# Kernel tuning notes

Hardware: AMD Instinct MI355X
Metric: run time of the kernel (lower is better)

## Reference

```python
import jax, jax.numpy as jnp
import numpy as np

B, C, F_IN = 262144, 4, 4   # batch, num label nodes, feature dim
HID = 64                     # hidden_dim (MLP embedding dim / GCN input)
GCN_H, GCN_OUT = 32, 4
EPS = 1e-8                   # torch F.cosine_similarity eps


def _glorot(k, shape):
    lim = float(np.sqrt(6.0 / (shape[0] + shape[1])))
    return jax.random.uniform(k, shape, jnp.float32, -lim, lim)


def setup_inputs() -> dict:
    key = jax.random.key(0)
    ks = jax.random.split(key, 7)
    return dict(
        x=jax.random.normal(ks[0], (B, C, F_IN), jnp.float32),
        # LabelEmbeddingMLP: 4 -> 128 -> 64 -> HID
        W1=_glorot(ks[1], (F_IN, 128)), b1=jnp.zeros((128,), jnp.float32),
        W2=_glorot(ks[2], (128, 64)),   b2=jnp.zeros((64,), jnp.float32),
        W3=_glorot(ks[3], (64, HID)),   b3=jnp.zeros((HID,), jnp.float32),
        # GCNModel: GCNConv(HID,32) -> GCNConv(32,4)
        Wg1=_glorot(ks[4], (HID, GCN_H)), bg1=jnp.zeros((GCN_H,), jnp.float32),
        Wg2=_glorot(ks[5], (GCN_H, GCN_OUT)), bg2=jnp.zeros((GCN_OUT,), jnp.float32),
    )


def reference(x, W1, b1, W2, b2, W3, b3, Wg1, bg1, Wg2, bg2):
    # --- label embedding MLP (applied per node) ---
    h = jax.nn.relu(x @ W1 + b1)
    h = jax.nn.relu(h @ W2 + b2)
    emb = h @ W3 + b3                                    # [B, C, HID]

    # --- per-sample cosine similarity, thresholded, unioned over batch ---
    # (the torch code keeps adding edges to ONE nx.Graph across all k, so the
    #  resulting 4-node edge set is the union over the batch; edge weights are
    #  ignored because GCNConv is called without edge_weight)
    n = x / jnp.maximum(jnp.linalg.norm(x, axis=-1, keepdims=True), EPS)
    sim = jnp.einsum('bif,bjf->bij', n, n)               # [B, C, C]
    adj = (sim > 0.5).any(axis=0) & ~jnp.eye(C, dtype=bool)
    adj = adj | adj.T

    # --- GCN normalized adjacency with self-loops: D^-1/2 (A+I) D^-1/2 ---
    A = adj.astype(jnp.float32) + jnp.eye(C, dtype=jnp.float32)
    dinv = jax.lax.rsqrt(A.sum(axis=1))
    Ahat = jax.lax.stop_gradient(dinv[:, None] * A * dinv[None, :])  # graph built via .item() is detached in torch

    # --- two GCNConv layers, shared Ahat broadcast over batch ---
    g = jax.nn.relu(jnp.einsum('ij,bjh->bih', Ahat, emb @ Wg1) + bg1)  # [B, C, 32]
    out = jnp.einsum('ij,bjh->bih', Ahat, g @ Wg2) + bg2               # [B, C, 4]
    return emb, out
```

## Files before the change

### kernel.cpp

```cpp
#include <hip/hip_runtime.h>

#define NB 262144
#define NNODE (NB * 4)
#define EMB_ELEMS ((size_t)NNODE * 64)
#define ADJ_BLOCKS (NNODE / 256)

typedef __attribute__((ext_vector_type(8))) _Float16 f16x8;
typedef __attribute__((ext_vector_type(4))) float f32x4;
typedef __attribute__((ext_vector_type(4))) unsigned int u32x4;

#define OW1E  0
#define OW2T  10240
#define OW3T  27648
#define OW3GT 36864
#define OWG2A 41472
#define OF32  42752
#define IMG_BYTES 43600
#define FB2   0
#define FB3   64
#define FB3G  128
#define FBG1  160
#define FBG2  192
#define FAHAT 196

#define NWAVE 8
#define WBUF_BYTES 4096
#define SMEM_BYTES (IMG_BYTES + NWAVE * WBUF_BYTES)

__device__ __forceinline__ int kperm(int ji) {
    int kt = ji >> 5, r = ji & 31, g = r >> 3, e = r & 7;
    return kt * 32 + ((e >> 2) << 4) + (g << 2) + (e & 3);
}

template <int J>
__device__ __forceinline__ float qb(float v) {
    constexpr int ctrl = J | (J << 2) | (J << 4) | (J << 6);
    int r = __builtin_amdgcn_update_dpp(0, __builtin_bit_cast(int, v), ctrl, 0xF, 0xF, true);
    return __builtin_bit_cast(float, r);
}

__global__ __launch_bounds__(256) void adj_kernel(const float* __restrict__ x,
                                                  unsigned int* __restrict__ mask_arr) {
    __shared__ unsigned int smask;
    if (threadIdx.x == 0) smask = 0u;
    __syncthreads();

    const int t = blockIdx.x * 256 + threadIdx.x;
    const int c = t & 3;
    f32x4 v = *(const f32x4*)(x + (size_t)t * 4);
    float nn = sqrtf(v.x * v.x + v.y * v.y + v.z * v.z + v.w * v.w);
    float inv = 1.0f / fmaxf(nn, 1e-8f);

    unsigned int m = 0u;
#define DOTJ(J) do {                                                            \
        const float bx = qb<J>(v.x), by = qb<J>(v.y);                           \
        const float bz = qb<J>(v.z), bw = qb<J>(v.w);                           \
        const float bi = qb<J>(inv);                                            \
        const float d = v.x * bx + v.y * by + v.z * bz + v.w * bw;              \
        if ((int)((J) != c) & (int)(d * inv * bi > 0.5f)) {                     \
            const int i_ = c < (J) ? c : (J);                                   \
            const int j_ = c < (J) ? (J) : c;                                   \
            m |= 1u << (2 * i_ + j_ - 1 - (i_ >> 1));                           \
        }                                                                       \
    } while (0)
    DOTJ(0); DOTJ(1); DOTJ(2); DOTJ(3);
#undef DOTJ

    if (m) atomicOr(&smask, m);
    __syncthreads();
    if (threadIdx.x == 0) mask_arr[blockIdx.x] = smask;
}

__global__ __launch_bounds__(256) void prep_kernel(
    const float* __restrict__ W1, const float* __restrict__ b1,
    const float* __restrict__ W2, const float* __restrict__ b2,
    const float* __restrict__ W3, const float* __restrict__ b3,
    const float* __restrict__ Wg1, const float* __restrict__ bg1,
    const float* __restrict__ Wg2, const float* __restrict__ bg2,
    const unsigned int* __restrict__ mask_arr, char* __restrict__ img)
{
    const int t = threadIdx.x;
    const int bid = blockIdx.x;
    _Float16* H = (_Float16*)img;
    float* F = (float*)(img + OF32);

    if (bid == 0) {
        __shared__ unsigned red[256];
        unsigned um = 0u;
        for (int i = t; i < ADJ_BLOCKS; i += 256) um |= mask_arr[i];
        red[t] = um;
        __syncthreads();
        for (int s = 128; s > 0; s >>= 1) {
            if (t < s) red[t] |= red[t + s];
            __syncthreads();
        }
        const unsigned m = red[0];

        for (int i = t; i < 64; i += 256) F[FB2 + i] = b2[i];
        for (int i = t; i < 64; i += 256) F[FB3 + i] = b3[i];
        for (int i = t; i < 32; i += 256) {
            float s = 0.f;
            for (int h = 0; h < 64; ++h) s = fmaf(b3[h], Wg1[h * 32 + i], s);
            F[FB3G + i] = s;
        }
        for (int i = t; i < 32; i += 256) F[FBG1 + i] = bg1[i];
        for (int i = t; i < 4; i += 256) F[FBG2 + i] = bg2[i];
        for (int i = t; i < 16 * 40; i += 256) {
            int o = i / 40, ji = i % 40;
            float v = (o < 4 && ji < 32) ? Wg2[kperm(ji) * 4 + o] : 0.f;
            H[OWG2A / 2 + i] = (_Float16)v;
        }
        if (t == 0) {
            float A[4][4];
            for (int i = 0; i < 4; ++i)
                for (int j = 0; j < 4; ++j) A[i][j] = (i == j) ? 1.f : 0.f;
            int bit = 0;
            for (int i = 0; i < 4; ++i)
                for (int j = i + 1; j < 4; ++j) {
                    if ((m >> bit) & 1u) { A[i][j] = 1.f; A[j][i] = 1.f; }
                    ++bit;
                }
            float dinv[4];
            for (int i = 0; i < 4; ++i)
                dinv[i] = 1.0f / sqrtf(A[i][0] + A[i][1] + A[i][2] + A[i][3]);
            for (int i = 0; i < 4; ++i)
                for (int j = 0; j < 4; ++j) F[FAHAT + i * 4 + j] = dinv[i] * A[i][j] * dinv[j];
        }
    } else if (bid == 1) {
        for (int i = t; i < 128 * 40; i += 256) {
            int j = i / 40, kk = i % 40;
            float v = (kk < 4) ? W1[kk * 128 + j] : (kk == 4 ? b1[j] : 0.f);
            H[OW1E / 2 + i] = (_Float16)v;
        }
    } else if (bid == 2) {
        for (int i = t; i < 64 * 136; i += 256) {
            int jo = i / 136, ji = i % 136;
            float v = 0.f;
            if (ji < 128) v = W2[kperm(ji) * 64 + jo];
            H[OW2T / 2 + i] = (_Float16)v;
        }
    } else {
        for (int i = t; i < 64 * 72; i += 256) {
            int h = i / 72, j = i % 72;
            float v = 0.f;
            if (j < 64) v = W3[kperm(j) * 64 + h];
            H[OW3T / 2 + i] = (_Float16)v;
        }
        for (int i = t; i < 32 * 72; i += 256) {
            int e = i / 72, j = i % 72;
            float s = 0.f;
            if (j < 64) {
                const int jj = kperm(j);
                for (int h = 0; h < 64; ++h) s = fmaf(W3[jj * 64 + h], Wg1[h * 32 + e], s);
            }
            H[OW3GT / 2 + i] = (_Float16)s;
        }
    }
}

__device__ __forceinline__ unsigned pkf16(float a, float b) {
    unsigned short ha = __builtin_bit_cast(unsigned short, (_Float16)a);
    unsigned short hb = __builtin_bit_cast(unsigned short, (_Float16)b);
    return (unsigned)ha | ((unsigned)hb << 16);
}
__device__ __forceinline__ f32x4 MF(f16x8 a, f16x8 b, f32x4 c) {
    return __builtin_amdgcn_mfma_f32_16x16x32_f16(a, b, c, 0, 0, 0);
}
__device__ __forceinline__ f16x8 ldA(const _Float16* p) {
    return *(const f16x8*)p;
}
__device__ __forceinline__ f16x8 bcat(unsigned X0, unsigned X1,
                                      unsigned Y0, unsigned Y1) {
    u32x4 t; t.x = X0; t.y = X1; t.z = Y0; t.w = Y1;
    return __builtin_bit_cast(f16x8, t);
}

__global__ __launch_bounds__(512, 2) void mlp_gcn_mfma(
    const float* __restrict__ x, const char* __restrict__ img,
    float* __restrict__ emb_out, float* __restrict__ out_out)
{
    __shared__ u32x4 smem4[SMEM_BYTES / 16];
    char* smem = (char*)smem4;
    const int tx = threadIdx.x;
    {
        const u32x4* src = (const u32x4*)img;
        u32x4* dst = (u32x4*)smem;
        for (int i = tx; i < IMG_BYTES / 16; i += 512) dst[i] = src[i];
    }
    __syncthreads();

    const _Float16* wh = (const _Float16*)smem;
    const float* wf = (const float*)(smem + OF32);

    const int wid = tx >> 6, lane = tx & 63;
    const int g = lane >> 4, c = lane & 15;
    const bool g0 = (g == 0);

    float* tb = (float*)(smem + IMG_BYTES) + wid * 1024;

    const f32x4 arow = *(const f32x4*)(wf + FAHAT + (c & 3) * 4);
    f32x4 bg1v[2];
    bg1v[0] = *(const f32x4*)(wf + FBG1 + g * 4);
    bg1v[1] = *(const f32x4*)(wf + FBG1 + 16 + g * 4);
    const f32x4 bg2v = *(const f32x4*)(wf + FBG2);
    const f16x8 aWg2 = ldA(wh + OWG2A / 2 + c * 40 + g * 8);

    const size_t nbase0 = ((size_t)blockIdx.x * NWAVE + wid) * 128;

#pragma unroll 1
    for (int it = 0; it < 2; ++it) {
        const size_t nbase = nbase0 + (size_t)it * 64;

        f16x8 xB[4];
#pragma unroll
        for (int nt = 0; nt < 4; ++nt) {
            f32x4 xq = *(const f32x4*)(x + (nbase + nt * 16 + c) * 4);
            u32x4 t;
            t.x = g0 ? pkf16(xq.x, xq.y) : 0u;
            t.y = g0 ? pkf16(xq.z, xq.w) : 0u;
            t.z = g0 ? 0x00003C00u : 0u;
            t.w = 0u;
            xB[nt] = __builtin_bit_cast(f16x8, t);
        }

        f32x4 acc2[4][4];
#pragma unroll
        for (int mt = 0; mt < 4; ++mt) {
            f32x4 bv = *(const f32x4*)(wf + FB2 + mt * 16 + g * 4);
#pragma unroll
            for (int nt = 0; nt < 4; ++nt) acc2[mt][nt] = bv;
        }
#pragma unroll
        for (int kt = 0; kt < 4; ++kt) {
            f16x8 a0 = ldA(wh + OW1E / 2 + ((2 * kt + 0) * 16 + c) * 40 + g * 8);
            f16x8 a1 = ldA(wh + OW1E / 2 + ((2 * kt + 1) * 16 + c) * 40 + g * 8);
            f16x8 bf[4];
#pragma unroll
            for (int nt = 0; nt < 4; ++nt) {
                f32x4 z = {0.f, 0.f, 0.f, 0.f};
                f32x4 t0 = MF(a0, xB[nt], z);
                f32x4 t1 = MF(a1, xB[nt], z);
                bf[nt] = bcat(pkf16(fmaxf(t0[0], 0.f), fmaxf(t0[1], 0.f)),
                              pkf16(fmaxf(t0[2], 0.f), fmaxf(t0[3], 0.f)),
                              pkf16(fmaxf(t1[0], 0.f), fmaxf(t1[1], 0.f)),
                              pkf16(fmaxf(t1[2], 0.f), fmaxf(t1[3], 0.f)));
            }
#pragma unroll
            for (int mt = 0; mt < 4; ++mt) {
                f16x8 a = ldA(wh + OW2T / 2 + (mt * 16 + c) * 136 + kt * 32 + g * 8);
#pragma unroll
                for (int nt = 0; nt < 4; ++nt) acc2[mt][nt] = MF(a, bf[nt], acc2[mt][nt]);
            }
        }

        unsigned pk2a[4][4][2];
#pragma unroll
        for (int mt = 0; mt < 4; ++mt)
#pragma unroll
            for (int nt = 0; nt < 4; ++nt) {
                pk2a[mt][nt][0] = pkf16(fmaxf(acc2[mt][nt][0], 0.f), fmaxf(acc2[mt][nt][1], 0.f));
                pk2a[mt][nt][1] = pkf16(fmaxf(acc2[mt][nt][2], 0.f), fmaxf(acc2[mt][nt][3], 0.f));
            }

        f32x4 acc3[4][4], acc4[2][4];
#pragma unroll
        for (int mt = 0; mt < 4; ++mt) {
            f32x4 bv = *(const f32x4*)(wf + FB3 + mt * 16 + g * 4);
#pragma unroll
            for (int nt = 0; nt < 4; ++nt) acc3[mt][nt] = bv;
        }
#pragma unroll
        for (int mt = 0; mt < 2; ++mt) {
            f32x4 bv = *(const f32x4*)(wf + FB3G + mt * 16 + g * 4);
#pragma unroll
            for (int nt = 0; nt < 4; ++nt) acc4[mt][nt] = bv;
        }
#pragma unroll
        for (int kt = 0; kt < 2; ++kt) {
            f16x8 bf[4];
#pragma unroll
            for (int nt = 0; nt < 4; ++nt)
                bf[nt] = bcat(pk2a[2 * kt][nt][0], pk2a[2 * kt][nt][1],
                              pk2a[2 * kt + 1][nt][0], pk2a[2 * kt + 1][nt][1]);
#pragma unroll
            for (int mt = 0; mt < 4; ++mt) {
                f16x8 a = ldA(wh + OW3T / 2 + (mt * 16 + c) * 72 + kt * 32 + g * 8);
#pragma unroll
                for (int nt = 0; nt < 4; ++nt) acc3[mt][nt] = MF(a, bf[nt], acc3[mt][nt]);
            }
#pragma unroll
            for (int mt = 0; mt < 2; ++mt) {
                f16x8 a = ldA(wh + OW3GT / 2 + (mt * 16 + c) * 72 + kt * 32 + g * 8);
#pragma unroll
                for (int nt = 0; nt < 4; ++nt) acc4[mt][nt] = MF(a, bf[nt], acc4[mt][nt]);
            }
        }

#pragma unroll
        for (int nt = 0; nt < 4; ++nt) {
            float gv[2][4];
#pragma unroll
            for (int m = 0; m < 2; ++m)
#pragma unroll
                for (int r = 0; r < 4; ++r) {
                    float v = acc4[m][nt][r];
                    float s = bg1v[m][r];
                    s = fmaf(arow.x, qb<0>(v), s);
                    s = fmaf(arow.y, qb<1>(v), s);
                    s = fmaf(arow.z, qb<2>(v), s);
                    s = fmaf(arow.w, qb<3>(v), s);
                    gv[m][r] = fmaxf(s, 0.f);
                }
            f16x8 bfg = bcat(pkf16(gv[0][0], gv[0][1]), pkf16(gv[0][2], gv[0][3]),
                             pkf16(gv[1][0], gv[1][1]), pkf16(gv[1][2], gv[1][3]));
            f32x4 z = {0.f, 0.f, 0.f, 0.f};
            f32x4 u4 = MF(aWg2, bfg, z);
            float ov[4];
#pragma unroll
            for (int o = 0; o < 4; ++o) {
                float s = bg2v[o];
                s = fmaf(arow.x, qb<0>(u4[o]), s);
                s = fmaf(arow.y, qb<1>(u4[o]), s);
                s = fmaf(arow.z, qb<2>(u4[o]), s);
                s = fmaf(arow.w, qb<3>(u4[o]), s);
                ov[o] = s;
            }
            if (g0) {
                f32x4 t; t.x = ov[0]; t.y = ov[1]; t.z = ov[2]; t.w = ov[3];
                *(f32x4*)(out_out + (nbase + nt * 16 + c) * 4) = t;
            }
        }

#pragma unroll
        for (int nt = 0; nt < 4; ++nt) {
#pragma unroll
            for (int mt = 0; mt < 4; ++mt) {
                int sl = (mt * 4 + g) ^ (c & 7);
                *(f32x4*)(tb + c * 64 + sl * 4) = acc3[mt][nt];
            }
            float* gp = emb_out + (nbase + nt * 16) * 64;
#pragma unroll
            for (int s = 0; s < 4; ++s) {
                int row = s * 4 + g;
                int sl = c ^ (row & 7);
                f32x4 q = *(const f32x4*)(tb + row * 64 + sl * 4);
                *(f32x4*)(gp + s * 256 + lane * 4) = q;
            }
        }
    }
}

extern "C" void kernel_launch(void* const* d_in, const int* in_sizes, int n_in,
                              void* d_out, int out_size, void* d_ws, size_t ws_size,
                              hipStream_t stream) {
    const float* x   = (const float*)d_in[0];
    const float* W1  = (const float*)d_in[1];
    const float* b1  = (const float*)d_in[2];
    const float* W2  = (const float*)d_in[3];
    const float* b2  = (const float*)d_in[4];
    const float* W3  = (const float*)d_in[5];
    const float* b3  = (const float*)d_in[6];
    const float* Wg1 = (const float*)d_in[7];
    const float* bg1 = (const float*)d_in[8];
    const float* Wg2 = (const float*)d_in[9];
    const float* bg2 = (const float*)d_in[10];

    unsigned int* mask_arr = (unsigned int*)d_ws;
    char* img = (char*)d_ws + 16640;

    float* emb_out = (float*)d_out;
    float* out_out = emb_out + EMB_ELEMS;

    adj_kernel<<<ADJ_BLOCKS, 256, 0, stream>>>(x, mask_arr);
    prep_kernel<<<4, 256, 0, stream>>>(W1, b1, W2, b2, W3, b3, Wg1, bg1, Wg2, bg2,
                                       mask_arr, img);
    mlp_gcn_mfma<<<NNODE / 1024, 512, 0, stream>>>(x, img, emb_out, out_out);
}
```

Measured before the change: 111.8 us.

## Split layer-3 MFMA into halves to cut registers and double per-wave work

Restructures the final MLP layer and GCN head so that the GCN branch runs first and the W3 embedding output is computed in two 32-column halves. This shrinks live accumulator registers so more waves can be resident. The per-half transpose staging now writes 32-column rows with stride 36 and stores half-rows to global memory. Each wave also now processes 256 nodes over 4 iterations with half as many blocks, which amortises the shared-memory weight image load but reduces grid parallelism and makes each 128-byte half-row store less contiguous.

```diff
diff --git a/kernel.cpp b/kernel.cpp
--- a/kernel.cpp
+++ b/kernel.cpp
@@ -198,17 +198,10 @@
 
     float* tb = (float*)(smem + IMG_BYTES) + wid * 1024;
 
-    const f32x4 arow = *(const f32x4*)(wf + FAHAT + (c & 3) * 4);
-    f32x4 bg1v[2];
-    bg1v[0] = *(const f32x4*)(wf + FBG1 + g * 4);
-    bg1v[1] = *(const f32x4*)(wf + FBG1 + 16 + g * 4);
-    const f32x4 bg2v = *(const f32x4*)(wf + FBG2);
-    const f16x8 aWg2 = ldA(wh + OWG2A / 2 + c * 40 + g * 8);
-
-    const size_t nbase0 = ((size_t)blockIdx.x * NWAVE + wid) * 128;
+    const size_t nbase0 = ((size_t)blockIdx.x * NWAVE + wid) * 256;
 
 #pragma unroll 1
-    for (int it = 0; it < 2; ++it) {
+    for (int it = 0; it < 4; ++it) {
         const size_t nbase = nbase0 + (size_t)it * 64;
 
         f16x8 xB[4];
@@ -262,89 +255,108 @@
                 pk2a[mt][nt][1] = pkf16(fmaxf(acc2[mt][nt][2], 0.f), fmaxf(acc2[mt][nt][3], 0.f));
             }
 
-        f32x4 acc3[4][4], acc4[2][4];
-#pragma unroll
-        for (int mt = 0; mt < 4; ++mt) {
-            f32x4 bv = *(const f32x4*)(wf + FB3 + mt * 16 + g * 4);
-#pragma unroll
-            for (int nt = 0; nt < 4; ++nt) acc3[mt][nt] = bv;
-        }
-#pragma unroll
-        for (int mt = 0; mt < 2; ++mt) {
-            f32x4 bv = *(const f32x4*)(wf + FB3G + mt * 16 + g * 4);
-#pragma unroll
-            for (int nt = 0; nt < 4; ++nt) acc4[mt][nt] = bv;
-        }
-#pragma unroll
-        for (int kt = 0; kt < 2; ++kt) {
-            f16x8 bf[4];
-#pragma unroll
-            for (int nt = 0; nt < 4; ++nt)
-                bf[nt] = bcat(pk2a[2 * kt][nt][0], pk2a[2 * kt][nt][1],
-                              pk2a[2 * kt + 1][nt][0], pk2a[2 * kt + 1][nt][1]);
-#pragma unroll
-            for (int mt = 0; mt < 4; ++mt) {
-                f16x8 a = ldA(wh + OW3T / 2 + (mt * 16 + c) * 72 + kt * 32 + g * 8);
-#pragma unroll
-                for (int nt = 0; nt < 4; ++nt) acc3[mt][nt] = MF(a, bf[nt], acc3[mt][nt]);
-            }
+        {
+            f32x4 acc4[2][4];
 #pragma unroll
             for (int mt = 0; mt < 2; ++mt) {
-                f16x8 a = ldA(wh + OW3GT / 2 + (mt * 16 + c) * 72 + kt * 32 + g * 8);
-#pragma unroll
-                for (int nt = 0; nt < 4; ++nt) acc4[mt][nt] = MF(a, bf[nt], acc4[mt][nt]);
-            }
-        }
-
-#pragma unroll
-        for (int nt = 0; nt < 4; ++nt) {
-            float gv[2][4];
-#pragma unroll
-            for (int m = 0; m < 2; ++m)
-#pragma unroll
-                for (int r = 0; r < 4; ++r) {
-                    float v = acc4[m][nt][r];
-                    float s = bg1v[m][r];
-                    s = fmaf(arow.x, qb<0>(v), s);
-                    s = fmaf(arow.y, qb<1>(v), s);
-                    s = fmaf(arow.z, qb<2>(v), s);
-                    s = fmaf(arow.w, qb<3>(v), s);
-                    gv[m][r] = fmaxf(s, 0.f);
-                }
-            f16x8 bfg = bcat(pkf16(gv[0][0], gv[0][1]), pkf16(gv[0][2], gv[0][3]),
-                             pkf16(gv[1][0], gv[1][1]), pkf16(gv[1][2], gv[1][3]));
-            f32x4 z = {0.f, 0.f, 0.f, 0.f};
-            f32x4 u4 = MF(aWg2, bfg, z);
-            float ov[4];
-#pragma unroll
-            for (int o = 0; o < 4; ++o) {
-                float s = bg2v[o];
-                s = fmaf(arow.x, qb<0>(u4[o]), s);
-                s = fmaf(arow.y, qb<1>(u4[o]), s);
-                s = fmaf(arow.z, qb<2>(u4[o]), s);
-                s = fmaf(arow.w, qb<3>(u4[o]), s);
-                ov[o] = s;
-            }
-            if (g0) {
-                f32x4 t; t.x = ov[0]; t.y = ov[1]; t.z = ov[2]; t.w = ov[3];
-                *(f32x4*)(out_out + (nbase + nt * 16 + c) * 4) = t;
-            }
-        }
-
-#pragma unroll
-        for (int nt = 0; nt < 4; ++nt) {
-#pragma unroll
-            for (int mt = 0; mt < 4; ++mt) {
-                int sl = (mt * 4 + g) ^ (c & 7);
-                *(f32x4*)(tb + c * 64 + sl * 4) = acc3[mt][nt];
-            }
-            float* gp = emb_out + (nbase + nt * 16) * 64;
-#pragma unroll
-            for (int s = 0; s < 4; ++s) {
-                int row = s * 4 + g;
-                int sl = c ^ (row & 7);
-                f32x4 q = *(const f32x4*)(tb + row * 64 + sl * 4);
-                *(f32x4*)(gp + s * 256 + lane * 4) = q;
+                f32x4 bv = *(const f32x4*)(wf + FB3G + mt * 16 + g * 4);
+#pragma unroll
+                for (int nt = 0; nt < 4; ++nt) acc4[mt][nt] = bv;
+            }
+#pragma unroll
+            for (int kt = 0; kt < 2; ++kt) {
+#pragma unroll
+                for (int mt = 0; mt < 2; ++mt) {
+                    f16x8 a = ldA(wh + OW3GT / 2 + (mt * 16 + c) * 72 + kt * 32 + g * 8);
+#pragma unroll
+                    for (int nt = 0; nt < 4; ++nt) {
+                        f16x8 bf = bcat(pk2a[2 * kt][nt][0], pk2a[2 * kt][nt][1],
+                                        pk2a[2 * kt + 1][nt][0], pk2a[2 * kt + 1][nt][1]);
+                        acc4[mt][nt] = MF(a, bf, acc4[mt][nt]);
+                    }
+                }
+            }
+            const f32x4 arow = *(const f32x4*)(wf + FAHAT + (c & 3) * 4);
+            f32x4 bg1v[2];
+            bg1v[0] = *(const f32x4*)(wf + FBG1 + g * 4);
+            bg1v[1] = *(const f32x4*)(wf + FBG1 + 16 + g * 4);
+            const f32x4 bg2v = *(const f32x4*)(wf + FBG2);
+            const f16x8 aWg2 = ldA(wh + OWG2A / 2 + c * 40 + g * 8);
+#pragma unroll
+            for (int nt = 0; nt < 4; ++nt) {
+                float gv[2][4];
+#pragma unroll
+                for (int m = 0; m < 2; ++m)
+#pragma unroll
+                    for (int r = 0; r < 4; ++r) {
+                        float v = acc4[m][nt][r];
+                        float s = bg1v[m][r];
+                        s = fmaf(arow.x, qb<0>(v), s);
+                        s = fmaf(arow.y, qb<1>(v), s);
+                        s = fmaf(arow.z, qb<2>(v), s);
+                        s = fmaf(arow.w, qb<3>(v), s);
+                        gv[m][r] = fmaxf(s, 0.f);
+                    }
+                f16x8 bfg = bcat(pkf16(gv[0][0], gv[0][1]), pkf16(gv[0][2], gv[0][3]),
+                                 pkf16(gv[1][0], gv[1][1]), pkf16(gv[1][2], gv[1][3]));
+                f32x4 z = {0.f, 0.f, 0.f, 0.f};
+                f32x4 u4 = MF(aWg2, bfg, z);
+                float ov[4];
+#pragma unroll
+                for (int o = 0; o < 4; ++o) {
+                    float s = bg2v[o];
+                    s = fmaf(arow.x, qb<0>(u4[o]), s);
+                    s = fmaf(arow.y, qb<1>(u4[o]), s);
+                    s = fmaf(arow.z, qb<2>(u4[o]), s);
+                    s = fmaf(arow.w, qb<3>(u4[o]), s);
+                    ov[o] = s;
+                }
+                if (g0) {
+                    f32x4 t; t.x = ov[0]; t.y = ov[1]; t.z = ov[2]; t.w = ov[3];
+                    *(f32x4*)(out_out + (nbase + nt * 16 + c) * 4) = t;
+                }
+            }
+        }
+
+#pragma unroll 1
+        for (int mh = 0; mh < 2; ++mh) {
+            f32x4 acc3h[2][4];
+#pragma unroll
+            for (int mt2 = 0; mt2 < 2; ++mt2) {
+                f32x4 bv = *(const f32x4*)(wf + FB3 + (mh * 2 + mt2) * 16 + g * 4);
+#pragma unroll
+                for (int nt = 0; nt < 4; ++nt) acc3h[mt2][nt] = bv;
+            }
+#pragma unroll
+            for (int kt = 0; kt < 2; ++kt) {
+#pragma unroll
+                for (int mt2 = 0; mt2 < 2; ++mt2) {
+                    const int mt = mh * 2 + mt2;
+                    f16x8 a = ldA(wh + OW3T / 2 + (mt * 16 + c) * 72 + kt * 32 + g * 8);
+#pragma unroll
+                    for (int nt = 0; nt < 4; ++nt) {
+                        f16x8 bf = bcat(pk2a[2 * kt][nt][0], pk2a[2 * kt][nt][1],
+                                        pk2a[2 * kt + 1][nt][0], pk2a[2 * kt + 1][nt][1]);
+                        acc3h[mt2][nt] = MF(a, bf, acc3h[mt2][nt]);
+                    }
+                }
+            }
+#pragma unroll
+            for (int nt = 0; nt < 4; ++nt) {
+#pragma unroll
+                for (int mt2 = 0; mt2 < 2; ++mt2) {
+                    int sl = (mt2 * 4 + g) ^ (c & 7);
+                    *(f32x4*)(tb + c * 36 + sl * 4) = acc3h[mt2][nt];
+                }
+                float* gp = emb_out + (nbase + nt * 16) * 64 + mh * 32;
+#pragma unroll
+                for (int s = 0; s < 2; ++s) {
+                    int F = s * 64 + lane;
+                    int node = F >> 3, col4 = F & 7;
+                    int sl = col4 ^ (node & 7);
+                    f32x4 q = *(const f32x4*)(tb + node * 36 + sl * 4);
+                    *(f32x4*)(gp + node * 64 + col4 * 4) = q;
+                }
             }
         }
     }
@@ -374,5 +386,5 @@
     adj_kernel<<<ADJ_BLOCKS, 256, 0, stream>>>(x, mask_arr);
     prep_kernel<<<4, 256, 0, stream>>>(W1, b1, W2, b2, W3, b3, Wg1, bg1, Wg2, bg2,
                                        mask_arr, img);
-    mlp_gcn_mfma<<<NNODE / 1024, 512, 0, stream>>>(x, img, emb_out, out_out);
-}
+    mlp_gcn_mfma<<<NNODE / 2048, 512, 0, stream>>>(x, img, emb_out, out_out);
+}
```

New measurement: 108.5 us. -2.9%, faster.
